# Kernel optimization log

Hardware: AMD Instinct MI355X
Metric: run time of the kernel (lower is better)

Reference implementation:

```python
import jax, jax.numpy as jnp
import numpy as np

B, D, U = 8192, 1024, 1024


def setup_inputs() -> dict:
    key = jax.random.key(0)
    ks = jax.random.split(key, 11)
    scale = 0.05  # keras 'random_normal' initializer default stddev
    inp = {
        "inputs": jax.random.normal(ks[0], (B, D), jnp.float32),
        "h_tm1": jax.random.normal(ks[1], (B, U), jnp.float32),
        "c_tm1": jax.random.normal(ks[2], (B, U), jnp.float32),
        "W_i": jax.random.normal(ks[3], (D, U), jnp.float32) * scale,
        "U_i": jax.random.normal(ks[4], (U, U), jnp.float32) * scale,
        "b_i": jnp.zeros((U,), jnp.float32),
        "W_f": jax.random.normal(ks[5], (D, U), jnp.float32) * scale,
        "U_f": jax.random.normal(ks[6], (U, U), jnp.float32) * scale,
        "b_f": jnp.zeros((U,), jnp.float32),
        "W_c": jax.random.normal(ks[7], (D, U), jnp.float32) * scale,
        "U_c": jax.random.normal(ks[8], (U, U), jnp.float32) * scale,
        "b_c": jnp.zeros((U,), jnp.float32),
        "W_o": jax.random.normal(ks[9], (D, U), jnp.float32) * scale,
        "U_o": jax.random.normal(ks[10], (U, U), jnp.float32) * scale,
        "b_o": jnp.zeros((U,), jnp.float32),
    }
    return inp


def reference(inputs, h_tm1, c_tm1, W_i, U_i, b_i, W_f, U_f, b_f, W_c, U_c, b_c, W_o, U_o, b_o):
    # Concatenate the 4 gate projections into single GEMMs (same math, fused form)
    Wx = jnp.concatenate([W_i, W_f, W_c, W_o], axis=1)  # [D, 4U]
    Uh = jnp.concatenate([U_i, U_f, U_c, U_o], axis=1)  # [U, 4U]
    b = jnp.concatenate([b_i, b_f, b_c, b_o], axis=0)   # [4U]
    z = inputs @ Wx + h_tm1 @ Uh + b                     # [B, 4U]
    u = W_i.shape[1]
    zi, zf, zc, zo = z[:, :u], z[:, u:2 * u], z[:, 2 * u:3 * u], z[:, 3 * u:]
    i = jax.nn.sigmoid(zi)
    f = jax.nn.sigmoid(zf)
    c_ = jnp.tanh(zc)
    c = f * c_tm1 + i * c_
    o = jax.nn.sigmoid(zo)
    h = o * jnp.tanh(c)
    return (h, c)
```

## Files before the change

kernel.cpp:

```cpp
#include <hip/hip_runtime.h>
#include <hip/hip_bf16.h>
#include <cstdint>


using f32x4  = __attribute__((ext_vector_type(4))) float;
using short8 = __attribute__((ext_vector_type(8))) short;

__device__ __forceinline__ unsigned short f2bf(float f) {
  union { float f; unsigned int u; } v; v.f = f;
  unsigned int r = v.u + 0x7fffu + ((v.u >> 16) & 1u);
  return (unsigned short)(r >> 16);
}
__device__ __forceinline__ float sigmoidf_fast(float x) { return 1.f / (1.f + __expf(-x)); }
__device__ __forceinline__ float tanhf_fast(float x)    { return 1.f - 2.f / (__expf(2.f * x) + 1.f); }

__global__ void conv_a_kernel(const float* __restrict__ X, const float* __restrict__ H,
                              unsigned short* __restrict__ Abf) {
  int idx = blockIdx.x * blockDim.x + threadIdx.x;
  int b  = idx >> 8;
  int kq = (idx & 255) << 2;
  float4 x = *(const float4*)(X + (long)b * 1024 + kq);
  float4 h = *(const float4*)(H + (long)b * 1024 + kq);
  ushort4 xo, ho;
  xo.x = f2bf(x.x); xo.y = f2bf(x.y); xo.z = f2bf(x.z); xo.w = f2bf(x.w);
  ho.x = f2bf(h.x); ho.y = f2bf(h.y); ho.z = f2bf(h.z); ho.w = f2bf(h.w);
  *(ushort4*)(Abf + (long)b * 2048 + kq)        = xo;
  *(ushort4*)(Abf + (long)b * 2048 + 1024 + kq) = ho;
}

__global__ void conv_b_kernel(const float* W_i, const float* U_i,
                              const float* W_f, const float* U_f,
                              const float* W_c, const float* U_c,
                              const float* W_o, const float* U_o,
                              unsigned short* __restrict__ Bt) {
  __shared__ float tile[64][65];
  int z = blockIdx.z;
  const float* src;
  switch (z) {
    case 0: src = W_i; break; case 1: src = U_i; break;
    case 2: src = W_f; break; case 3: src = U_f; break;
    case 4: src = W_c; break; case 5: src = U_c; break;
    case 6: src = W_o; break; default: src = U_o; break;
  }
  int g = z >> 1, s = z & 1;
  int k0 = blockIdx.x * 64;
  int u0 = blockIdx.y * 64;
  int t = threadIdx.x;
  int c = t & 63, r0 = t >> 6;
#pragma unroll
  for (int i = 0; i < 16; ++i) {
    int r = i * 4 + r0;
    tile[r][c] = src[(long)(k0 + r) * 1024 + u0 + c];
  }
  __syncthreads();
  int ul = t >> 2;
  int ks = (t & 3) * 16;
  unsigned short outv[16];
#pragma unroll
  for (int j = 0; j < 16; ++j) outv[j] = f2bf(tile[ks + j][ul]);
  long n   = 4L * u0 + (ul >> 4) * 64 + g * 16 + (ul & 15);
  long col = (long)s * 1024 + k0 + ks;
  uint4* dst = (uint4*)(Bt + n * 2048 + col);
  dst[0] = *(uint4*)(outv);
  dst[1] = *(uint4*)(outv + 8);
}

__global__ __launch_bounds__(512, 2) void lstm_gemm_kernel(
    const unsigned short* __restrict__ Abf,
    const unsigned short* __restrict__ Btbf,
    const float* __restrict__ b_i, const float* __restrict__ b_f,
    const float* __restrict__ b_c, const float* __restrict__ b_o,
    const float* __restrict__ c_tm1,
    float* __restrict__ outH, float* __restrict__ outC) {
  __shared__ unsigned short smem[65536];

  int bid = blockIdx.x;
  int swz = (bid & 7) * 64 + (bid >> 3);
  int bm = swz >> 4;
  int bn = swz & 15;

  int t = threadIdx.x;
  int lane = t & 63;
  int w = t >> 6;
  int wm = w >> 2;
  int wn = w & 3;
  int rl = lane & 15;
  int kg = lane >> 4;

#define AOFFE(MI) ((wm * 128 + (MI) * 16 + rl) * 32 + \
    ((kg ^ (((wm * 128 + (MI) * 16 + rl) >> 1) & 3)) << 3))
#define BOFFE(NI) ((wn * 64 + (NI) * 16 + rl) * 32 + \
    ((kg ^ (((wn * 64 + (NI) * 16 + rl) >> 1) & 3)) << 3))
  const int offA0 = AOFFE(0), offA1 = AOFFE(1), offA2 = AOFFE(2), offA3 = AOFFE(3);
  const int offA4 = AOFFE(4), offA5 = AOFFE(5), offA6 = AOFFE(6), offA7 = AOFFE(7);
  const int offB0 = BOFFE(0), offB1 = BOFFE(1), offB2 = BOFFE(2), offB3 = BOFFE(3);
#undef AOFFE
#undef BOFFE

  int srow = t >> 2;
  int ks   = (t & 3) ^ ((srow >> 1) & 3);
  const unsigned short* aS0 = Abf  + (long)(bm * 256 + srow) * 2048 + ks * 8;
  const unsigned short* aS1 = aS0 + 128L * 2048;
  const unsigned short* bS0 = Btbf + (long)(bn * 256 + srow) * 2048 + ks * 8;
  const unsigned short* bS1 = bS0 + 128L * 2048;
  const int dA = t * 8;

#define GLL(SRC, DELM)                                                                     \
  __builtin_amdgcn_global_load_lds((const __attribute__((address_space(1))) void*)(SRC),   \
      (__attribute__((address_space(3))) void*)(&smem[DELM]), 16, 0, 0)

#define STAGE_A(SD, SKH, KOFF)                                                 \
  do {                                                                         \
    GLL(aS0 + (KOFF), (SD) * 16384 + (SKH) * 8192 + dA);                       \
    GLL(aS1 + (KOFF), (SD) * 16384 + (SKH) * 8192 + 4096 + dA);                \
  } while (0)
#define STAGE_B(SD, SKH, KOFF)                                                 \
  do {                                                                         \
    GLL(bS0 + (KOFF), 32768 + (SD) * 16384 + (SKH) * 8192 + dA);               \
    GLL(bS1 + (KOFF), 32768 + (SD) * 16384 + (SKH) * 8192 + 4096 + dA);        \
  } while (0)
#define VMC(N) asm volatile("s_waitcnt vmcnt(" #N ")" ::: "memory")

  f32x4 acc[8][4];
#pragma unroll
  for (int mi = 0; mi < 8; ++mi)
#pragma unroll
    for (int ni = 0; ni < 4; ++ni) acc[mi][ni] = (f32x4){0.f, 0.f, 0.f, 0.f};

  short8 aw0, aw1, aw2, aw3, bb0, bb1, bb2, bb3;

#define MF4(AF, MI)                                                                      \
  acc[MI][0] = __builtin_amdgcn_mfma_f32_16x16x32_bf16(AF, bb0, acc[MI][0], 0, 0, 0);    \
  acc[MI][1] = __builtin_amdgcn_mfma_f32_16x16x32_bf16(AF, bb1, acc[MI][1], 0, 0, 0);    \
  acc[MI][2] = __builtin_amdgcn_mfma_f32_16x16x32_bf16(AF, bb2, acc[MI][2], 0, 0, 0);    \
  acc[MI][3] = __builtin_amdgcn_mfma_f32_16x16x32_bf16(AF, bb3, acc[MI][3], 0, 0, 0);

#define PH_MH0(D, KK, STG, VM)                                                 \
  {                                                                            \
    const unsigned short* Ab_ = smem + (D) * 16384 + (KK) * 8192;              \
    const unsigned short* Bb_ = smem + 32768 + (D) * 16384 + (KK) * 8192;      \
    aw0 = *(const short8*)(Ab_ + offA0);                                       \
    aw1 = *(const short8*)(Ab_ + offA1);                                       \
    aw2 = *(const short8*)(Ab_ + offA2);                                       \
    aw3 = *(const short8*)(Ab_ + offA3);                                       \
    bb0 = *(const short8*)(Bb_ + offB0);                                       \
    bb1 = *(const short8*)(Bb_ + offB1);                                       \
    bb2 = *(const short8*)(Bb_ + offB2);                                       \
    bb3 = *(const short8*)(Bb_ + offB3);                                       \
    STG;                                                                       \
    __builtin_amdgcn_s_barrier();                                              \
    asm volatile("s_waitcnt lgkmcnt(0)" ::: "memory");                         \
    __builtin_amdgcn_sched_barrier(0);                                         \
    __builtin_amdgcn_s_setprio(1);                                             \
    MF4(aw0, 0) MF4(aw1, 1) MF4(aw2, 2) MF4(aw3, 3)                            \
    __builtin_amdgcn_s_setprio(0);                                             \
    VM;                                                                        \
    __builtin_amdgcn_s_barrier();                                              \
  }

#define PH_MH1(D, KK, STG, VM)                                                 \
  {                                                                            \
    const unsigned short* Ab_ = smem + (D) * 16384 + (KK) * 8192;              \
    aw0 = *(const short8*)(Ab_ + offA4);                                       \
    aw1 = *(const short8*)(Ab_ + offA5);                                       \
    aw2 = *(const short8*)(Ab_ + offA6);                                       \
    aw3 = *(const short8*)(Ab_ + offA7);                                       \
    STG;                                                                       \
    __builtin_amdgcn_s_barrier();                                              \
    asm volatile("s_waitcnt lgkmcnt(0)" ::: "memory");                         \
    __builtin_amdgcn_sched_barrier(0);                                         \
    __builtin_amdgcn_s_setprio(1);                                             \
    MF4(aw0, 4) MF4(aw1, 5) MF4(aw2, 6) MF4(aw3, 7)                            \
    __builtin_amdgcn_s_setprio(0);                                             \
    VM;                                                                        \
    __builtin_amdgcn_s_barrier();                                              \
  }

  STAGE_A(0, 0, 0);  STAGE_B(0, 0, 0);
  STAGE_A(0, 1, 32); STAGE_B(0, 1, 32);
  STAGE_A(1, 0, 64); STAGE_B(1, 0, 64);
  STAGE_A(1, 1, 96); STAGE_B(1, 1, 96);
  VMC(8);
  __builtin_amdgcn_s_barrier();

  PH_MH0(0, 0, (void)0,             (void)0);
  PH_MH1(0, 0, (void)0,             VMC(8));
  PH_MH0(0, 1, STAGE_A(0, 0, 128),  (void)0);
  PH_MH1(0, 1, STAGE_B(0, 0, 128),  VMC(8));
  PH_MH0(1, 0, STAGE_A(0, 1, 160),  (void)0);
  PH_MH1(1, 0, STAGE_B(0, 1, 160),  VMC(8));
  PH_MH0(1, 1, STAGE_A(1, 0, 192),  (void)0);
  PH_MH1(1, 1, STAGE_B(1, 0, 192),  VMC(8));
  aS0 += 128; aS1 += 128; bS0 += 128; bS1 += 128;

  for (int i = 1; i <= 14; ++i) {
    PH_MH0(0, 0, STAGE_A(1, 1, 96),   (void)0);
    PH_MH1(0, 0, STAGE_B(1, 1, 96),   VMC(8));
    PH_MH0(0, 1, STAGE_A(0, 0, 128),  (void)0);
    PH_MH1(0, 1, STAGE_B(0, 0, 128),  VMC(8));
    PH_MH0(1, 0, STAGE_A(0, 1, 160),  (void)0);
    PH_MH1(1, 0, STAGE_B(0, 1, 160),  VMC(8));
    PH_MH0(1, 1, STAGE_A(1, 0, 192),  (void)0);
    PH_MH1(1, 1, STAGE_B(1, 0, 192),  VMC(8));
    aS0 += 128; aS1 += 128; bS0 += 128; bS1 += 128;
  }

  PH_MH0(0, 0, STAGE_A(1, 1, 96),   (void)0);
  PH_MH1(0, 0, STAGE_B(1, 1, 96),   VMC(8));
  PH_MH0(0, 1, (void)0,             (void)0);
  PH_MH1(0, 1, (void)0,             VMC(4));
  PH_MH0(1, 0, (void)0,             (void)0);
  PH_MH1(1, 0, (void)0,             VMC(0));
  PH_MH0(1, 1, (void)0,             (void)0);
  PH_MH1(1, 1, (void)0,             (void)0);

#undef PH_MH0
#undef PH_MH1
#undef MF4
#undef VMC
#undef STAGE_A
#undef STAGE_B
#undef GLL

  int mbase = bm * 256 + wm * 128;
  int nbase = bn * 256 + wn * 64;
  int u = (nbase >> 2) + rl;
  float bi_v = b_i[u], bf_v = b_f[u], bc_v = b_c[u], bo_v = b_o[u];
  int rquad = (lane >> 4) << 2;
#pragma unroll
  for (int mi = 0; mi < 8; ++mi) {
#pragma unroll
    for (int j = 0; j < 4; ++j) {
      int brow = mbase + mi * 16 + rquad + j;
      float zi = acc[mi][0][j] + bi_v;
      float zf = acc[mi][1][j] + bf_v;
      float zc = acc[mi][2][j] + bc_v;
      float zo = acc[mi][3][j] + bo_v;
      float ig = sigmoidf_fast(zi);
      float fg = sigmoidf_fast(zf);
      float cg = tanhf_fast(zc);
      float og = sigmoidf_fast(zo);
      float cp = c_tm1[(long)brow * 1024 + u];
      float cn = fg * cp + ig * cg;
      float hn = og * tanhf_fast(cn);
      outH[(long)brow * 1024 + u] = hn;
      outC[(long)brow * 1024 + u] = cn;
    }
  }
}

extern "C" void kernel_launch(void* const* d_in, const int* in_sizes, int n_in,
                              void* d_out, int out_size, void* d_ws, size_t ws_size,
                              hipStream_t stream) {
  (void)in_sizes; (void)n_in; (void)out_size; (void)ws_size;
  const float* X   = (const float*)d_in[0];
  const float* Hst = (const float*)d_in[1];
  const float* Cst = (const float*)d_in[2];
  const float* W_i = (const float*)d_in[3];
  const float* U_i = (const float*)d_in[4];
  const float* b_i = (const float*)d_in[5];
  const float* W_f = (const float*)d_in[6];
  const float* U_f = (const float*)d_in[7];
  const float* b_f = (const float*)d_in[8];
  const float* W_c = (const float*)d_in[9];
  const float* U_c = (const float*)d_in[10];
  const float* b_c = (const float*)d_in[11];
  const float* W_o = (const float*)d_in[12];
  const float* U_o = (const float*)d_in[13];
  const float* b_o = (const float*)d_in[14];

  unsigned short* Abf  = (unsigned short*)d_ws;
  unsigned short* Btbf = (unsigned short*)((char*)d_ws + 33554432);

  float* outH = (float*)d_out;
  float* outC = outH + 8192L * 1024;

  conv_a_kernel<<<8192, 256, 0, stream>>>(X, Hst, Abf);
  conv_b_kernel<<<dim3(16, 16, 8), 256, 0, stream>>>(W_i, U_i, W_f, U_f, W_c, U_c, W_o, U_o, Btbf);
  lstm_gemm_kernel<<<512, 512, 0, stream>>>(Abf, Btbf, b_i, b_f, b_c, b_o, Cst, outH, outC);
}
```

Baseline: 162.1 us.

## Restructure GEMM main loop into 3-stage ring with one barrier per window

```diff
diff --git a/kernel.cpp b/kernel.cpp
--- a/kernel.cpp
+++ b/kernel.cpp
@@ -72,7 +72,7 @@
     const float* __restrict__ b_c, const float* __restrict__ b_o,
     const float* __restrict__ c_tm1,
     float* __restrict__ outH, float* __restrict__ outC) {
-  __shared__ unsigned short smem[65536];
+  __shared__ unsigned short smem[49152];
 
   int bid = blockIdx.x;
   int swz = (bid & 7) * 64 + (bid >> 3);
@@ -89,7 +89,7 @@
 
 #define AOFFE(MI) ((wm * 128 + (MI) * 16 + rl) * 32 + \
     ((kg ^ (((wm * 128 + (MI) * 16 + rl) >> 1) & 3)) << 3))
-#define BOFFE(NI) ((wn * 64 + (NI) * 16 + rl) * 32 + \
+#define BOFFE(NI) (8192 + (wn * 64 + (NI) * 16 + rl) * 32 + \
     ((kg ^ (((wn * 64 + (NI) * 16 + rl) >> 1) & 3)) << 3))
   const int offA0 = AOFFE(0), offA1 = AOFFE(1), offA2 = AOFFE(2), offA3 = AOFFE(3);
   const int offA4 = AOFFE(4), offA5 = AOFFE(5), offA6 = AOFFE(6), offA7 = AOFFE(7);
@@ -98,27 +98,16 @@
 #undef BOFFE
 
   int srow = t >> 2;
-  int ks   = (t & 3) ^ ((srow >> 1) & 3);
-  const unsigned short* aS0 = Abf  + (long)(bm * 256 + srow) * 2048 + ks * 8;
+  int cbe  = (((t & 3) ^ ((srow >> 1) & 3))) << 3;
+  const unsigned short* aS0 = Abf  + (long)(bm * 256 + srow) * 2048 + cbe;
   const unsigned short* aS1 = aS0 + 128L * 2048;
-  const unsigned short* bS0 = Btbf + (long)(bn * 256 + srow) * 2048 + ks * 8;
+  const unsigned short* bS0 = Btbf + (long)(bn * 256 + srow) * 2048 + cbe;
   const unsigned short* bS1 = bS0 + 128L * 2048;
   const int dA = t * 8;
 
 #define GLL(SRC, DELM)                                                                     \
   __builtin_amdgcn_global_load_lds((const __attribute__((address_space(1))) void*)(SRC),   \
       (__attribute__((address_space(3))) void*)(&smem[DELM]), 16, 0, 0)
-
-#define STAGE_A(SD, SKH, KOFF)                                                 \
-  do {                                                                         \
-    GLL(aS0 + (KOFF), (SD) * 16384 + (SKH) * 8192 + dA);                       \
-    GLL(aS1 + (KOFF), (SD) * 16384 + (SKH) * 8192 + 4096 + dA);                \
-  } while (0)
-#define STAGE_B(SD, SKH, KOFF)                                                 \
-  do {                                                                         \
-    GLL(bS0 + (KOFF), 32768 + (SD) * 16384 + (SKH) * 8192 + dA);               \
-    GLL(bS1 + (KOFF), 32768 + (SD) * 16384 + (SKH) * 8192 + 4096 + dA);        \
-  } while (0)
 #define VMC(N) asm volatile("s_waitcnt vmcnt(" #N ")" ::: "memory")
 
   f32x4 acc[8][4];
@@ -135,91 +124,61 @@
   acc[MI][2] = __builtin_amdgcn_mfma_f32_16x16x32_bf16(AF, bb2, acc[MI][2], 0, 0, 0);    \
   acc[MI][3] = __builtin_amdgcn_mfma_f32_16x16x32_bf16(AF, bb3, acc[MI][3], 0, 0, 0);
 
-#define PH_MH0(D, KK, STG, VM)                                                 \
+#define WINDOW(RB, SB, KOFF, DOSTAGE, VMN, DOBAR)                              \
   {                                                                            \
-    const unsigned short* Ab_ = smem + (D) * 16384 + (KK) * 8192;              \
-    const unsigned short* Bb_ = smem + 32768 + (D) * 16384 + (KK) * 8192;      \
+    const unsigned short* Ab_ = smem + (RB) * 16384;                           \
+    bb0 = *(const short8*)(Ab_ + offB0);                                       \
+    bb1 = *(const short8*)(Ab_ + offB1);                                       \
+    bb2 = *(const short8*)(Ab_ + offB2);                                       \
+    bb3 = *(const short8*)(Ab_ + offB3);                                       \
     aw0 = *(const short8*)(Ab_ + offA0);                                       \
     aw1 = *(const short8*)(Ab_ + offA1);                                       \
     aw2 = *(const short8*)(Ab_ + offA2);                                       \
     aw3 = *(const short8*)(Ab_ + offA3);                                       \
-    bb0 = *(const short8*)(Bb_ + offB0);                                       \
-    bb1 = *(const short8*)(Bb_ + offB1);                                       \
-    bb2 = *(const short8*)(Bb_ + offB2);                                       \
-    bb3 = *(const short8*)(Bb_ + offB3);                                       \
-    STG;                                                                       \
-    __builtin_amdgcn_s_barrier();                                              \
-    asm volatile("s_waitcnt lgkmcnt(0)" ::: "memory");                         \
-    __builtin_amdgcn_sched_barrier(0);                                         \
+    if (DOSTAGE) {                                                             \
+      GLL(aS0 + (KOFF), (SB) * 16384 + dA);                                    \
+      GLL(aS1 + (KOFF), (SB) * 16384 + 4096 + dA);                             \
+    }                                                                          \
     __builtin_amdgcn_s_setprio(1);                                             \
     MF4(aw0, 0) MF4(aw1, 1) MF4(aw2, 2) MF4(aw3, 3)                            \
     __builtin_amdgcn_s_setprio(0);                                             \
-    VM;                                                                        \
-    __builtin_amdgcn_s_barrier();                                              \
-  }
-
-#define PH_MH1(D, KK, STG, VM)                                                 \
-  {                                                                            \
-    const unsigned short* Ab_ = smem + (D) * 16384 + (KK) * 8192;              \
     aw0 = *(const short8*)(Ab_ + offA4);                                       \
     aw1 = *(const short8*)(Ab_ + offA5);                                       \
     aw2 = *(const short8*)(Ab_ + offA6);                                       \
     aw3 = *(const short8*)(Ab_ + offA7);                                       \
-    STG;                                                                       \
-    __builtin_amdgcn_s_barrier();                                              \
-    asm volatile("s_waitcnt lgkmcnt(0)" ::: "memory");                         \
-    __builtin_amdgcn_sched_barrier(0);                                         \
+    if (DOSTAGE) {                                                             \
+      GLL(bS0 + (KOFF), (SB) * 16384 + 8192 + dA);                             \
+      GLL(bS1 + (KOFF), (SB) * 16384 + 12288 + dA);                            \
+    }                                                                          \
     __builtin_amdgcn_s_setprio(1);                                             \
     MF4(aw0, 4) MF4(aw1, 5) MF4(aw2, 6) MF4(aw3, 7)                            \
     __builtin_amdgcn_s_setprio(0);                                             \
-    VM;                                                                        \
-    __builtin_amdgcn_s_barrier();                                              \
-  }
-
-  STAGE_A(0, 0, 0);  STAGE_B(0, 0, 0);
-  STAGE_A(0, 1, 32); STAGE_B(0, 1, 32);
-  STAGE_A(1, 0, 64); STAGE_B(1, 0, 64);
-  STAGE_A(1, 1, 96); STAGE_B(1, 1, 96);
-  VMC(8);
+    if ((VMN) == 4) VMC(4);                                                    \
+    if ((VMN) == 0) VMC(0);                                                    \
+    if (DOBAR) __builtin_amdgcn_s_barrier();                                   \
+  }
+
+  GLL(aS0, dA);            GLL(aS1, 4096 + dA);
+  GLL(bS0, 8192 + dA);     GLL(bS1, 12288 + dA);
+  GLL(aS0 + 32, 16384 + dA);        GLL(aS1 + 32, 16384 + 4096 + dA);
+  GLL(bS0 + 32, 16384 + 8192 + dA); GLL(bS1 + 32, 16384 + 12288 + dA);
+  VMC(4);
   __builtin_amdgcn_s_barrier();
-
-  PH_MH0(0, 0, (void)0,             (void)0);
-  PH_MH1(0, 0, (void)0,             VMC(8));
-  PH_MH0(0, 1, STAGE_A(0, 0, 128),  (void)0);
-  PH_MH1(0, 1, STAGE_B(0, 0, 128),  VMC(8));
-  PH_MH0(1, 0, STAGE_A(0, 1, 160),  (void)0);
-  PH_MH1(1, 0, STAGE_B(0, 1, 160),  VMC(8));
-  PH_MH0(1, 1, STAGE_A(1, 0, 192),  (void)0);
-  PH_MH1(1, 1, STAGE_B(1, 0, 192),  VMC(8));
-  aS0 += 128; aS1 += 128; bS0 += 128; bS1 += 128;
-
-  for (int i = 1; i <= 14; ++i) {
-    PH_MH0(0, 0, STAGE_A(1, 1, 96),   (void)0);
-    PH_MH1(0, 0, STAGE_B(1, 1, 96),   VMC(8));
-    PH_MH0(0, 1, STAGE_A(0, 0, 128),  (void)0);
-    PH_MH1(0, 1, STAGE_B(0, 0, 128),  VMC(8));
-    PH_MH0(1, 0, STAGE_A(0, 1, 160),  (void)0);
-    PH_MH1(1, 0, STAGE_B(0, 1, 160),  VMC(8));
-    PH_MH0(1, 1, STAGE_A(1, 0, 192),  (void)0);
-    PH_MH1(1, 1, STAGE_B(1, 0, 192),  VMC(8));
-    aS0 += 128; aS1 += 128; bS0 += 128; bS1 += 128;
-  }
-
-  PH_MH0(0, 0, STAGE_A(1, 1, 96),   (void)0);
-  PH_MH1(0, 0, STAGE_B(1, 1, 96),   VMC(8));
-  PH_MH0(0, 1, (void)0,             (void)0);
-  PH_MH1(0, 1, (void)0,             VMC(4));
-  PH_MH0(1, 0, (void)0,             (void)0);
-  PH_MH1(1, 0, (void)0,             VMC(0));
-  PH_MH0(1, 1, (void)0,             (void)0);
-  PH_MH1(1, 1, (void)0,             (void)0);
-
-#undef PH_MH0
-#undef PH_MH1
+  aS0 += 64; aS1 += 64; bS0 += 64; bS1 += 64;
+
+  for (int g = 0; g < 20; ++g) {
+    WINDOW(0, 2, 0,  1, 4, 1);
+    WINDOW(1, 0, 32, 1, 4, 1);
+    WINDOW(2, 1, 64, 1, 4, 1);
+    aS0 += 96; aS1 += 96; bS0 += 96; bS1 += 96;
+  }
+  WINDOW(0, 2, 0,  1, 4, 1);
+  WINDOW(1, 0, 32, 1, 4, 1);
+  WINDOW(2, 0, 0,  0, 0, 1);
+  WINDOW(0, 0, 0,  0, -1, 0);
+#undef WINDOW
 #undef MF4
 #undef VMC
-#undef STAGE_A
-#undef STAGE_B
 #undef GLL
 
   int mbase = bm * 256 + wm * 128;
```

New measurement: 159.7 us. Within noise of the previous version (-1.5%).
